# Kernel tuning notes

Measured on AMD Instinct MI355X. Metric: run time of the kernel, lower is better.

The kernel has to match this reference:

```python
import jax, jax.numpy as jnp
import numpy as np

B = 262144
X_DIM = 40
N_FEAT = 18


def setup_inputs() -> dict:
    key = jax.random.key(0)
    k_u, k_c = jax.random.split(key)
    u = jax.random.normal(k_u, (B, X_DIM), dtype=jnp.float32)
    coeff = jax.random.normal(k_c, (N_FEAT,), dtype=jnp.float32) * 0.1
    return {"t": 0, "u": u, "coeff": coeff}


def reference(t, u, coeff):
    # circular shifts along last (state) axis; u_m2[i] = u[(i-2) % n] == roll(+2)
    u_m2 = jnp.roll(u, 2, axis=-1)
    u_m1 = jnp.roll(u, 1, axis=-1)
    u_p1 = jnp.roll(u, -1, axis=-1)
    u_p2 = jnp.roll(u, -2, axis=-1)
    feats = jnp.stack([
        jnp.ones_like(u),
        u_m2, u_m1, u, u_p1, u_p2,
        u_m2 * u_m2, u_m1 * u_m1, u * u, u_p1 * u_p1, u_p2 * u_p2,
        u_m2 * u_m1, u_m1 * u, u * u_p1, u_p1 * u_p2,
        u_m2 * u, u_m1 * u_p1, u * u_p2,
    ], axis=-1)  # (B, X_DIM, 18)
    return feats @ coeff  # (B, X_DIM)
```

## Files before the change

### kernel.cpp

```cpp
#include <hip/hip_runtime.h>

#define XDIM 40
#define VPR 10

__global__ __launch_bounds__(256) void lorenz96_feats_kernel(
    const float4* __restrict__ u4,
    const float* __restrict__ coeff,
    float4* __restrict__ out4,
    int total_vec) {
    int v = blockIdx.x * blockDim.x + threadIdx.x;
    if (v >= total_vec) return;

    unsigned int uv = (unsigned int)v;
    unsigned int r  = uv / VPR;
    unsigned int p4 = uv - r * VPR;

    const float4* row = u4 + (size_t)r * VPR;
    float4 cen = row[p4];
    float4 prv = row[p4 == 0        ? VPR - 1 : p4 - 1];
    float4 nxt = row[p4 == VPR - 1  ? 0       : p4 + 1];

    float a[8];
    a[0] = prv.z; a[1] = prv.w;
    a[2] = cen.x; a[3] = cen.y; a[4] = cen.z; a[5] = cen.w;
    a[6] = nxt.x; a[7] = nxt.y;

    float c0  = coeff[0],  c1  = coeff[1],  c2  = coeff[2],  c3  = coeff[3];
    float c4  = coeff[4],  c5  = coeff[5],  c6  = coeff[6],  c7  = coeff[7];
    float c8  = coeff[8],  c9  = coeff[9],  c10 = coeff[10], c11 = coeff[11];
    float c12 = coeff[12], c13 = coeff[13], c14 = coeff[14], c15 = coeff[15];
    float c16 = coeff[16], c17 = coeff[17];

    float o[4];
    #pragma unroll
    for (int k = 0; k < 4; ++k) {
        float um2 = a[k];
        float um1 = a[k + 1];
        float uc  = a[k + 2];
        float up1 = a[k + 3];
        float up2 = a[k + 4];
        float val = c0
            + um2 * (c1 + c6 * um2 + c11 * um1 + c15 * uc)
            + um1 * (c2 + c7 * um1 + c12 * uc  + c16 * up1)
            + uc  * (c3 + c8 * uc  + c13 * up1 + c17 * up2)
            + up1 * (c4 + c9 * up1 + c14 * up2)
            + up2 * (c5 + c10 * up2);
        o[k] = val;
    }

    float4 ov;
    ov.x = o[0]; ov.y = o[1]; ov.z = o[2]; ov.w = o[3];
    out4[v] = ov;
}

extern "C" void kernel_launch(void* const* d_in, const int* in_sizes, int n_in,
                              void* d_out, int out_size, void* d_ws, size_t ws_size,
                              hipStream_t stream) {
    const float* u     = (const float*)d_in[1];
    const float* coeff = (const float*)d_in[2];
    float*       out   = (float*)d_out;

    int total_vec = out_size / 4;
    int blocks    = (total_vec + 255) / 256;
    lorenz96_feats_kernel<<<blocks, 256, 0, stream>>>(
        (const float4*)u, coeff, (float4*)out, total_vec);
}
```

Measured before the change: 96.45 us.

## Process one full row per thread to eliminate redundant neighbor loads

Each thread now loads an entire 40-element row into registers and computes all 40 outputs, instead of one float4 with two neighbor float4 loads. This removes the redundant neighbor reads and the division used for indexing. In exchange, memory accesses within a wavefront become strided by a full row, which hurts coalescing, and per-thread register use rises.

```diff
diff --git a/kernel.cpp b/kernel.cpp
--- a/kernel.cpp
+++ b/kernel.cpp
@@ -3,27 +3,23 @@
 #define XDIM 40
 #define VPR 10
 
-__global__ __launch_bounds__(256) void lorenz96_feats_kernel(
+__global__ __launch_bounds__(256) void lorenz96_row_kernel(
     const float4* __restrict__ u4,
     const float* __restrict__ coeff,
     float4* __restrict__ out4,
-    int total_vec) {
-    int v = blockIdx.x * blockDim.x + threadIdx.x;
-    if (v >= total_vec) return;
+    int rows) {
+    int r = blockIdx.x * blockDim.x + threadIdx.x;
+    if (r >= rows) return;
 
-    unsigned int uv = (unsigned int)v;
-    unsigned int r  = uv / VPR;
-    unsigned int p4 = uv - r * VPR;
+    const float4* __restrict__ row  = u4   + (size_t)r * VPR;
+    float4* __restrict__       orow = out4 + (size_t)r * VPR;
 
-    const float4* row = u4 + (size_t)r * VPR;
-    float4 cen = row[p4];
-    float4 prv = row[p4 == 0        ? VPR - 1 : p4 - 1];
-    float4 nxt = row[p4 == VPR - 1  ? 0       : p4 + 1];
-
-    float a[8];
-    a[0] = prv.z; a[1] = prv.w;
-    a[2] = cen.x; a[3] = cen.y; a[4] = cen.z; a[5] = cen.w;
-    a[6] = nxt.x; a[7] = nxt.y;
+    float a[XDIM];
+    #pragma unroll
+    for (int i = 0; i < VPR; ++i) {
+        float4 b = row[i];
+        a[4*i+0] = b.x; a[4*i+1] = b.y; a[4*i+2] = b.z; a[4*i+3] = b.w;
+    }
 
     float c0  = coeff[0],  c1  = coeff[1],  c2  = coeff[2],  c3  = coeff[3];
     float c4  = coeff[4],  c5  = coeff[5],  c6  = coeff[6],  c7  = coeff[7];
@@ -31,26 +27,28 @@
     float c12 = coeff[12], c13 = coeff[13], c14 = coeff[14], c15 = coeff[15];
     float c16 = coeff[16], c17 = coeff[17];
 
-    float o[4];
     #pragma unroll
-    for (int k = 0; k < 4; ++k) {
-        float um2 = a[k];
-        float um1 = a[k + 1];
-        float uc  = a[k + 2];
-        float up1 = a[k + 3];
-        float up2 = a[k + 4];
-        float val = c0
-            + um2 * (c1 + c6 * um2 + c11 * um1 + c15 * uc)
-            + um1 * (c2 + c7 * um1 + c12 * uc  + c16 * up1)
-            + uc  * (c3 + c8 * uc  + c13 * up1 + c17 * up2)
-            + up1 * (c4 + c9 * up1 + c14 * up2)
-            + up2 * (c5 + c10 * up2);
-        o[k] = val;
+    for (int i = 0; i < VPR; ++i) {
+        float o[4];
+        #pragma unroll
+        for (int k = 0; k < 4; ++k) {
+            const int idx = 4*i + k;
+            const float um2 = a[(idx + XDIM - 2) % XDIM];
+            const float um1 = a[(idx + XDIM - 1) % XDIM];
+            const float uc  = a[idx];
+            const float up1 = a[(idx + 1) % XDIM];
+            const float up2 = a[(idx + 2) % XDIM];
+            o[k] = c0
+                + um2 * (c1 + c6  * um2 + c11 * um1 + c15 * uc)
+                + um1 * (c2 + c7  * um1 + c12 * uc  + c16 * up1)
+                + uc  * (c3 + c8  * uc  + c13 * up1 + c17 * up2)
+                + up1 * (c4 + c9  * up1 + c14 * up2)
+                + up2 * (c5 + c10 * up2);
+        }
+        float4 ov;
+        ov.x = o[0]; ov.y = o[1]; ov.z = o[2]; ov.w = o[3];
+        orow[i] = ov;
     }
-
-    float4 ov;
-    ov.x = o[0]; ov.y = o[1]; ov.z = o[2]; ov.w = o[3];
-    out4[v] = ov;
 }
 
 extern "C" void kernel_launch(void* const* d_in, const int* in_sizes, int n_in,
@@ -60,8 +58,8 @@
     const float* coeff = (const float*)d_in[2];
     float*       out   = (float*)d_out;
 
-    int total_vec = out_size / 4;
-    int blocks    = (total_vec + 255) / 256;
-    lorenz96_feats_kernel<<<blocks, 256, 0, stream>>>(
-        (const float4*)u, coeff, (float4*)out, total_vec);
+    int rows   = out_size / XDIM;
+    int blocks = (rows + 255) / 256;
+    lorenz96_row_kernel<<<blocks, 256, 0, stream>>>(
+        (const float4*)u, coeff, (float4*)out, rows);
 }
```

New measurement: 111.5 us. +15.6%, slower.
